# Optimization experiments

Hardware: AMD Instinct MI355X
Metric: run time of the kernel (lower is better)

Reference implementation:

```python
import jax, jax.numpy as jnp
import numpy as np

NUM_GAUSS = 64
MAX_R = 5.0
ANG_TO_NM = 0.1  # du.ANG_TO_NM_SCALE
L = 4
C_NODE = 256
C_HID = 256
MAX_ATOMS = 100
B = 512      # building blocks
NPB = 32     # atoms per block
K = 20       # max_neighbors
N = B * NPB
E = N * K
GAUSS_COEFF = -0.5 / (MAX_R / (NUM_GAUSS - 1)) ** 2


def setup_inputs() -> dict:
    rng = np.random.default_rng(0)
    # all atoms of a block inside a 2.5A cube -> every pair within MAX_R=5A,
    # so radius_graph capped at K neighbors == K-nearest graph (fixed E).
    pos = (rng.random((B, NPB, 3)) * 2.5).astype(np.float32)
    d = np.linalg.norm(pos[:, :, None, :] - pos[:, None, :, :], axis=-1)  # [B,n,n]
    ii = np.arange(NPB)
    d[:, ii, ii] = np.inf  # loop=False
    nbr = np.argsort(d, axis=-1)[:, :, :K]  # [B,n,K] nearest neighbors
    base = (np.arange(B) * NPB)[:, None, None]
    row = np.broadcast_to(ii[None, :, None], (B, NPB, K)) + base
    col = nbr + base
    edge_index = np.stack([row.reshape(-1), col.reshape(-1)]).astype(np.int64)

    key = jax.random.key(0)
    ks = jax.random.split(key, 8)

    def lin(k, fi, fo):
        return jax.random.normal(k, (L, fi, fo), jnp.float32) / np.sqrt(fi).astype(np.float32)

    d_e_in = 2 * C_NODE + 1 + NUM_GAUSS  # 577
    return {
        'local_coords': jnp.asarray(pos.reshape(N, 3)),
        'atom_types': jax.random.randint(ks[0], (N,), 1, MAX_ATOMS + 1),  # 1..max_atoms
        'edge_index': jnp.asarray(edge_index),
        'batch_bb': jnp.repeat(jnp.arange(B, dtype=jnp.int32), NPB),
        'atom_embed': jax.random.normal(ks[1], (MAX_ATOMS, C_NODE), jnp.float32) * 0.1,
        'offset': jnp.linspace(0.0, MAX_R, NUM_GAUSS, dtype=jnp.float32),
        'We1': lin(ks[2], d_e_in, C_HID), 'be1': jnp.zeros((L, C_HID), jnp.float32),
        'We2': lin(ks[3], C_HID, C_HID), 'be2': jnp.zeros((L, C_HID), jnp.float32),
        'Wn1': lin(ks[4], C_HID + C_NODE, C_HID), 'bn1': jnp.zeros((L, C_HID), jnp.float32),
        'Wn2': lin(ks[5], C_HID, C_NODE), 'bn2': jnp.zeros((L, C_NODE), jnp.float32),
    }


def _forward(local_coords, atom_types, edge_index, batch_bb, atom_embed, offset,
             We1, be1, We2, be2, Wn1, bn1, Wn2, bn2):
    row, col = edge_index[0], edge_index[1]
    h = atom_embed[atom_types - 1]                      # [N, C_NODE]
    # Gaussian smearing of pairwise distances (Angstrom)
    dvec = local_coords[col] - local_coords[row]        # [E, 3]
    dist = jnp.sqrt(jnp.sum(dvec * dvec, axis=-1))      # [E]
    edge_attr = jnp.exp(GAUSS_COEFF * (dist[:, None] - offset[None, :]) ** 2)  # [E, 64]
    coord = local_coords * ANG_TO_NM
    cdiff = coord[row] - coord[col]
    radial = jnp.sum(cdiff * cdiff, axis=-1, keepdims=True)  # [E, 1]
    nblocks = batch_bb.shape[0] // NPB  # static
    for l in range(L):  # small fixed layer count
        e_in = jnp.concatenate([h[row], h[col], radial, edge_attr], axis=-1)  # [E, 577]
        m = jax.nn.relu(e_in @ We1[l] + be1[l])
        m = jax.nn.relu(m @ We2[l] + be2[l])                 # edge_mlp output [E, C_HID]
        agg = jax.ops.segment_sum(m, row, num_segments=N)    # scatter-sum to nodes
        n_in = jnp.concatenate([h, agg], axis=-1)            # [N, C_NODE + C_HID]
        out = jax.nn.relu(n_in @ Wn1[l] + bn1[l]) @ Wn2[l] + bn2[l]
        node_update = h + out                                # residual inside E_GCL
        h = h + node_update                                  # outer residual in forward
    # global_mean_pool over building blocks
    s = jax.ops.segment_sum(h, batch_bb, num_segments=B)
    cnt = jax.ops.segment_sum(jnp.ones((h.shape[0], 1), h.dtype), batch_bb, num_segments=B)
    return s / cnt


def reference(local_coords, atom_types, edge_index, batch_bb, atom_embed, offset,
              We1, be1, We2, be2, Wn1, bn1, Wn2, bn2):
    return _forward(local_coords, atom_types, edge_index, batch_bb, atom_embed, offset,
                    We1, be1, We2, be2, Wn1, bn1, Wn2, bn2)
```

## Files before the change

kernel.cpp:

```cpp
#include <hip/hip_runtime.h>
#include <hip/hip_bf16.h>
#include <stdint.h>

#define NATOMS 16384
#define ETOT   327680
#define NLAYER 4

typedef __hip_bfloat16 bf16;
using bf16x8 = __attribute__((ext_vector_type(8))) short;
using f32x4  = __attribute__((ext_vector_type(4))) float;

#define LDSF_STRIDE 260
#define WBR_STRIDE  66

__device__ __forceinline__ float bf2f(short s) {
  union { float f; unsigned u; } x; x.u = ((unsigned)(unsigned short)s) << 16; return x.f;
}
__device__ __forceinline__ short f2bf(float f) {
  bf16 b = __float2bfloat16(f);
  return *(short*)&b;
}

__device__ __forceinline__ void async16(const void* g, void* l) {
  __builtin_amdgcn_global_load_lds(
      (const __attribute__((address_space(1))) unsigned int*)g,
      (__attribute__((address_space(3))) unsigned int*)l, 16, 0, 0);
}

template<int KTOT, int EPI, int MT>
__global__ void __launch_bounds__(256, 2)
gemm_k(const bf16* A, const bf16* A2, const bf16* B,
       bf16* Obf, int ldOut, const float* bias,
       float* Hf, bf16* Hbf)
{
  __shared__ __align__(16) char smem[49152];
  __shared__ float s_bias[256];

  const int tid  = threadIdx.x;
  const int w    = tid >> 6;
  const int lane = tid & 63;
  const int q    = lane >> 4;
  const int t16  = lane & 15;
  const size_t row0 = (size_t)blockIdx.x * MT;
  const int ncol0 = blockIdx.y * 256;
  constexpr int MI = MT / 16;
  constexpr int AI = MT / 32;

  if constexpr (EPI == 2 || EPI == 4) s_bias[tid] = bias[tid];

  f32x4 acc[MI][4] = {};

  constexpr int NCHUNK = KTOT / 64;
  for (int kc = 0; kc < NCHUNK; ++kc) {
    const int k0 = kc * 64;
    const bf16* Asrc; int k0e; int ldA;
    if constexpr (KTOT == 512) {
      if (k0 < 256) { Asrc = A;  k0e = k0;       }
      else          { Asrc = A2; k0e = k0 - 256; }
      ldA = 256;
    } else {
      Asrc = A; k0e = k0; ldA = KTOT;
    }

    __syncthreads();
    #pragma unroll
    for (int ii = 0; ii < AI; ++ii) {
      int i = w * AI + ii;
      int f = i * 64 + lane;
      int m = f >> 3, s = f & 7;
      int ko = s ^ (m & 7);
      const bf16* g = Asrc + (row0 + (size_t)m) * ldA + (size_t)(k0e + ko * 8);
      async16(g, smem + i * 1024);
    }
    #pragma unroll
    for (int ii = 0; ii < 8; ++ii) {
      int i = w * 8 + ii;
      int f = i * 64 + lane;
      int n = f >> 3, s = f & 7;
      int ko = s ^ (n & 7);
      const bf16* g = B + (size_t)(ncol0 + n) * KTOT + (size_t)(k0 + ko * 8);
      async16(g, smem + 16384 + i * 1024);
    }
    __syncthreads();

    #pragma unroll
    for (int ks = 0; ks < 2; ++ks) {
      bf16x8 av[MI]; bf16x8 bv[4];
      const int ko = q + 4 * ks;
      #pragma unroll
      for (int mi = 0; mi < MI; ++mi) {
        int m = 16 * mi + t16;
        int f = m * 8 + (ko ^ (m & 7));
        av[mi] = *(const bf16x8*)(smem + f * 16);
      }
      #pragma unroll
      for (int ni = 0; ni < 4; ++ni) {
        int n = 64 * w + 16 * ni + t16;
        int f = n * 8 + (ko ^ (n & 7));
        bv[ni] = *(const bf16x8*)(smem + 16384 + f * 16);
      }
      #pragma unroll
      for (int mi = 0; mi < MI; ++mi)
        #pragma unroll
        for (int ni = 0; ni < 4; ++ni)
          acc[mi][ni] = __builtin_amdgcn_mfma_f32_16x16x32_bf16(
              av[mi], bv[ni], acc[mi][ni], 0, 0, 0);
    }
  }

  float* lds_f = (float*)smem;
  #pragma unroll
  for (int mi = 0; mi < MI; ++mi) {
    __syncthreads();
    #pragma unroll
    for (int ni = 0; ni < 4; ++ni)
      #pragma unroll
      for (int r = 0; r < 4; ++r)
        lds_f[(4 * q + r) * LDSF_STRIDE + 64 * w + 16 * ni + t16] = acc[mi][ni][r];
    __syncthreads();
    #pragma unroll
    for (int j = 0; j < 2; ++j) {
      int task = tid + 256 * j;
      int rr = task >> 5, cg = task & 31;
      int c0 = cg * 8;
      size_t rg = row0 + 16 * mi + rr;
      f32x4 v0 = *(const f32x4*)(lds_f + rr * LDSF_STRIDE + c0);
      f32x4 v1 = *(const f32x4*)(lds_f + rr * LDSF_STRIDE + c0 + 4);
      float v[8] = {v0[0], v0[1], v0[2], v0[3], v1[0], v1[1], v1[2], v1[3]};
      if constexpr (EPI == 0) {
        bf16x8 o;
        #pragma unroll
        for (int k = 0; k < 8; ++k) o[k] = f2bf(v[k]);
        *(bf16x8*)(Obf + rg * ldOut + (ncol0 + c0)) = o;
      } else if constexpr (EPI == 2) {
        bf16x8 o;
        #pragma unroll
        for (int k = 0; k < 8; ++k) o[k] = f2bf(fmaxf(v[k] + s_bias[c0 + k], 0.f));
        *(bf16x8*)(Obf + rg * 256 + c0) = o;
      } else {
        f32x4 h0 = *(const f32x4*)(Hf + rg * 256 + c0);
        f32x4 h1 = *(const f32x4*)(Hf + rg * 256 + c0 + 4);
        float hh[8] = {h0[0], h0[1], h0[2], h0[3], h1[0], h1[1], h1[2], h1[3]};
        bf16x8 o; f32x4 n0, n1;
        #pragma unroll
        for (int k = 0; k < 8; ++k) {
          float hn = 2.f * hh[k] + v[k] + s_bias[c0 + k];
          o[k] = f2bf(hn);
          if (k < 4) n0[k] = hn; else n1[k - 4] = hn;
        }
        *(f32x4*)(Hf + rg * 256 + c0)     = n0;
        *(f32x4*)(Hf + rg * 256 + c0 + 4) = n1;
        *(bf16x8*)(Hbf + rg * 256 + c0) = o;
      }
    }
  }
}

#define M1OFF 0
#define BREG  40960
__global__ void __launch_bounds__(256, 2)
edge_fused(const bf16* WgT_l, const bf16* We2T_l, const float* off,
           const float* pos, const int* eidx, const bf16* Prc,
           const float* be1, const float* wrad, const float* be2, bf16* Agg)
{
  __shared__ __align__(16) char smem[73728];
  __shared__ int   s_erow[80];
  __shared__ int   s_ecol[80];
  __shared__ float s_rad[80];
  __shared__ float s_dist[80];
  __shared__ float s_b1[256];
  __shared__ float s_wrad[256];
  __shared__ float s_b2[256];
  __shared__ float s_off[64];

  const int tid  = threadIdx.x;
  const int w    = tid >> 6;
  const int lane = tid & 63;
  const int q    = lane >> 4;
  const int t16  = lane & 15;
  const size_t erow0 = (size_t)blockIdx.x * 80;

  if (tid < 80) {
    int e = (int)erow0 + tid;
    int r = eidx[e], c = eidx[ETOT + e];
    float dx = pos[c * 3 + 0] - pos[r * 3 + 0];
    float dy = pos[c * 3 + 1] - pos[r * 3 + 1];
    float dz = pos[c * 3 + 2] - pos[r * 3 + 2];
    float d2 = dx * dx + dy * dy + dz * dz;
    s_erow[tid] = r; s_ecol[tid] = c;
    s_rad[tid]  = 0.01f * d2;
    s_dist[tid] = sqrtf(d2);
  }
  if (tid < 64) s_off[tid] = off[tid];
  s_b1[tid]   = be1[tid];
  s_wrad[tid] = wrad[tid];
  s_b2[tid]   = be2[tid];

  #pragma unroll
  for (int ii = 0; ii < 8; ++ii) {
    int i = w * 8 + ii;
    int f = i * 64 + lane;
    int n = f >> 3, s = f & 7;
    int ko = s ^ (n & 7);
    async16(WgT_l + (size_t)n * 64 + ko * 8, smem + BREG + i * 1024);
  }
  __syncthreads();

  const float GC = -0.5f / ((5.0f / 63.0f) * (5.0f / 63.0f));
  float offk[2][8];
  #pragma unroll
  for (int ks = 0; ks < 2; ++ks)
    #pragma unroll
    for (int j = 0; j < 8; ++j) offk[ks][j] = s_off[(q + 4 * ks) * 8 + j];

  bf16x8 ag[5][2];
  #pragma unroll
  for (int mi = 0; mi < 5; ++mi) {
    float d = s_dist[16 * mi + t16];
    #pragma unroll
    for (int ks = 0; ks < 2; ++ks)
      #pragma unroll
      for (int j = 0; j < 8; ++j) {
        float t = d - offk[ks][j];
        ag[mi][ks][j] = f2bf(__expf(GC * t * t));
      }
  }

  f32x4 acc1[5][4] = {};
  #pragma unroll
  for (int ks = 0; ks < 2; ++ks) {
    bf16x8 bv[4];
    const int ko = q + 4 * ks;
    #pragma unroll
    for (int ni = 0; ni < 4; ++ni) {
      int n = 64 * w + 16 * ni + t16;
      int f = n * 8 + (ko ^ (n & 7));
      bv[ni] = *(const bf16x8*)(smem + BREG + f * 16);
    }
    #pragma unroll
    for (int mi = 0; mi < 5; ++mi)
      #pragma unroll
      for (int ni = 0; ni < 4; ++ni)
        acc1[mi][ni] = __builtin_amdgcn_mfma_f32_16x16x32_bf16(
            ag[mi][ks], bv[ni], acc1[mi][ni], 0, 0, 0);
  }

  {
    float* br = (float*)(smem + BREG + 8192 * w);
    const int rs = lane >> 3, oct = lane & 7;
    const int c0e = 64 * w + oct * 8;
    float b18[8], wr8[8];
    #pragma unroll
    for (int k = 0; k < 8; ++k) { b18[k] = s_b1[c0e + k]; wr8[k] = s_wrad[c0e + k]; }

    #pragma unroll
    for (int mi = 0; mi < 5; ++mi) {
      #pragma unroll
      for (int ni = 0; ni < 4; ++ni)
        #pragma unroll
        for (int r = 0; r < 4; ++r)
          br[(4 * q + r) * WBR_STRIDE + 16 * ni + t16] = acc1[mi][ni][r];
      #pragma unroll
      for (int pass = 0; pass < 2; ++pass) {
        int rr = pass * 8 + rs;
        int rl = 16 * mi + rr;
        int er = s_erow[rl], ec = s_ecol[rl];
        float rad = s_rad[rl];
        bf16x8 pr = *(const bf16x8*)(Prc + (size_t)er * 512 + c0e);
        bf16x8 pc = *(const bf16x8*)(Prc + (size_t)ec * 512 + 256 + c0e);
        float v[8];
        #pragma unroll
        for (int jj = 0; jj < 4; ++jj) {
          float2 t = *(const float2*)(br + rr * WBR_STRIDE + oct * 8 + 2 * jj);
          v[2 * jj] = t.x; v[2 * jj + 1] = t.y;
        }
        bf16x8 o;
        #pragma unroll
        for (int k = 0; k < 8; ++k) {
          float val = v[k] + b18[k] + rad * wr8[k] + bf2f(pr[k]) + bf2f(pc[k]);
          o[k] = f2bf(fmaxf(val, 0.f));
        }
        int od = (8 * w + oct) ^ (rl & 7);
        *(bf16x8*)(smem + rl * 512 + od * 16) = o;
      }
    }
  }
  __syncthreads();

  f32x4 acc2[5][4] = {};
  for (int kc = 0; kc < 4; ++kc) {
    if (kc) __syncthreads();
    #pragma unroll
    for (int ii = 0; ii < 8; ++ii) {
      int i = w * 8 + ii;
      int f = i * 64 + lane;
      int n = f >> 3, s = f & 7;
      int ko = s ^ (n & 7);
      async16(We2T_l + (size_t)n * 256 + (size_t)(64 * kc + ko * 8),
              smem + BREG + i * 1024);
    }
    __syncthreads();

    #pragma unroll
    for (int ks = 0; ks < 2; ++ks) {
      bf16x8 av[5]; bf16x8 bv[4];
      const int ko = q + 4 * ks;
      #pragma unroll
      for (int mi = 0; mi < 5; ++mi) {
        int m = 16 * mi + t16;
        int oa = (8 * kc + ko) ^ (t16 & 7);
        av[mi] = *(const bf16x8*)(smem + m * 512 + oa * 16);
      }
      #pragma unroll
      for (int ni = 0; ni < 4; ++ni) {
        int n = 64 * w + 16 * ni + t16;
        int f = n * 8 + (ko ^ (n & 7));
        bv[ni] = *(const bf16x8*)(smem + BREG + f * 16);
      }
      #pragma unroll
      for (int mi = 0; mi < 5; ++mi)
        #pragma unroll
        for (int ni = 0; ni < 4; ++ni)
          acc2[mi][ni] = __builtin_amdgcn_mfma_f32_16x16x32_bf16(
              av[mi], bv[ni], acc2[mi][ni], 0, 0, 0);
    }
  }

  #pragma unroll
  for (int ni = 0; ni < 4; ++ni) {
    float b = s_b2[64 * w + 16 * ni + t16];
    float pp[5];
    #pragma unroll
    for (int mi = 0; mi < 5; ++mi) {
      float s = 0.f;
      #pragma unroll
      for (int r = 0; r < 4; ++r) s += fmaxf(acc2[mi][ni][r] + b, 0.f);
      pp[mi] = s;
    }
    #pragma unroll
    for (int nn = 0; nn < 4; ++nn) {
      float s = 0.f;
      #pragma unroll
      for (int mi = 0; mi < 5; ++mi) {
        int g = 4 * mi + q;
        if (g >= 5 * nn && g <= 5 * nn + 4) s += pp[mi];
      }
      s += __shfl_xor(s, 16, 64);
      s += __shfl_xor(s, 32, 64);
      if (q == nn)
        Agg[((size_t)blockIdx.x * 4 + nn) * 256 + 64 * w + 16 * ni + t16] =
            __float2bfloat16(s);
    }
  }
}

__global__ void wrct_kernel(const float* We1, bf16* WrcT) {
  int idx = blockIdx.x * 256 + threadIdx.x;
  int k = idx & 255, np = (idx >> 8) & 511, l = idx >> 17;
  float v = (np < 256)
      ? We1[((size_t)l * 577 + k) * 256 + np]
      : We1[((size_t)l * 577 + 256 + k) * 256 + (np - 256)];
  WrcT[idx] = __float2bfloat16(v);
}
__global__ void wgt_kernel(const float* We1, bf16* WgT) {
  int idx = blockIdx.x * 256 + threadIdx.x;
  int k = idx & 63, n = (idx >> 6) & 255, l = idx >> 14;
  WgT[idx] = __float2bfloat16(We1[((size_t)l * 577 + 513 + k) * 256 + n]);
}
__global__ void wrad_kernel(const float* We1, float* wrad) {
  int idx = blockIdx.x * 256 + threadIdx.x;
  int n = idx & 255, l = idx >> 8;
  wrad[idx] = We1[((size_t)l * 577 + 512) * 256 + n];
}
__global__ void trans_kernel(const float* src, bf16* dst, int R, int C) {
  int idx = blockIdx.x * 256 + threadIdx.x;
  int k = idx % R, rest = idx / R;
  int n = rest % C, l = rest / C;
  dst[idx] = __float2bfloat16(src[((size_t)l * R + k) * C + n]);
}

__global__ void h0_kernel(const int* types, const float* emb, float* h, bf16* hbf) {
  int i = blockIdx.x, c = threadIdx.x;
  float v = emb[(size_t)(types[i] - 1) * 256 + c];
  h[(size_t)i * 256 + c] = v;
  hbf[(size_t)i * 256 + c] = __float2bfloat16(v);
}

__global__ void pool_kernel(const float* h, float* out) {
  int b = blockIdx.x, c = threadIdx.x;
  float s = 0.f;
  #pragma unroll
  for (int j = 0; j < 32; ++j) s += h[((size_t)b * 32 + j) * 256 + c];
  out[(size_t)b * 256 + c] = s * (1.0f / 32.0f);
}

extern "C" void kernel_launch(void* const* d_in, const int* in_sizes, int n_in,
                              void* d_out, int out_size, void* d_ws, size_t ws_size,
                              hipStream_t stream) {
  const float* pos   = (const float*)d_in[0];
  const int*   atype = (const int*)  d_in[1];
  const int*   eidx  = (const int*)  d_in[2];
  const float* emb   = (const float*)d_in[4];
  const float* off   = (const float*)d_in[5];
  const float* We1   = (const float*)d_in[6];
  const float* be1   = (const float*)d_in[7];
  const float* We2   = (const float*)d_in[8];
  const float* be2   = (const float*)d_in[9];
  const float* Wn1   = (const float*)d_in[10];
  const float* bn1   = (const float*)d_in[11];
  const float* Wn2   = (const float*)d_in[12];
  const float* bn2   = (const float*)d_in[13];
  float* out = (float*)d_out;

  size_t o = 0;
  auto carve = [&](size_t bytes) {
    void* p = (char*)d_ws + o;
    o += (bytes + 255) & ~(size_t)255;
    return p;
  };
  float* h     = (float*)carve((size_t)NATOMS * 256 * 4);
  bf16*  hbf   = (bf16*) carve((size_t)NATOMS * 256 * 2);
  bf16*  Prc   = (bf16*) carve((size_t)NATOMS * 512 * 2);
  bf16*  aggbf = (bf16*) carve((size_t)NATOMS * 256 * 2);
  bf16*  WrcT  = (bf16*) carve((size_t)NLAYER * 512 * 256 * 2);
  bf16*  WgT   = (bf16*) carve((size_t)NLAYER * 256 * 64 * 2);
  bf16*  We2T  = (bf16*) carve((size_t)NLAYER * 256 * 256 * 2);
  bf16*  Wn1T  = (bf16*) carve((size_t)NLAYER * 256 * 512 * 2);
  bf16*  Wn2T  = (bf16*) carve((size_t)NLAYER * 256 * 256 * 2);
  float* wradp = (float*)carve((size_t)NLAYER * 256 * 4);

  wrct_kernel<<<2048, 256, 0, stream>>>(We1, WrcT);
  wgt_kernel <<< 256, 256, 0, stream>>>(We1, WgT);
  wrad_kernel<<<   4, 256, 0, stream>>>(We1, wradp);
  trans_kernel<<<1024, 256, 0, stream>>>(We2, We2T, 256, 256);
  trans_kernel<<<2048, 256, 0, stream>>>(Wn1, Wn1T, 512, 256);
  trans_kernel<<<1024, 256, 0, stream>>>(Wn2, Wn2T, 256, 256);
  h0_kernel  <<<NATOMS, 256, 0, stream>>>(atype, emb, h, hbf);

  for (int l = 0; l < NLAYER; ++l) {
    gemm_k<256, 0, 64><<<dim3(256, 2), 256, 0, stream>>>(
        hbf, nullptr, WrcT + (size_t)l * 512 * 256, Prc, 512, nullptr,
        nullptr, nullptr);
    edge_fused<<<ETOT / 80, 256, 0, stream>>>(
        WgT + (size_t)l * 256 * 64, We2T + (size_t)l * 256 * 256, off, pos,
        eidx, Prc, be1 + l * 256, wradp + l * 256, be2 + l * 256, aggbf);
    gemm_k<512, 2, 64><<<dim3(256, 1), 256, 0, stream>>>(
        hbf, aggbf, Wn1T + (size_t)l * 256 * 512, aggbf, 256, bn1 + l * 256,
        nullptr, nullptr);
    gemm_k<256, 4, 64><<<dim3(256, 1), 256, 0, stream>>>(
        aggbf, nullptr, Wn2T + (size_t)l * 256 * 256, nullptr, 0, bn2 + l * 256,
        h, hbf);
  }

  pool_kernel<<<512, 256, 0, stream>>>(h, out);
}
```

Baseline: 645.4 us.

## Load edge-MLP weights straight into registers and shrink LDS for higher occupancy

The edge_fused kernel stops staging the Gaussian weight matrix and the We2 tiles through LDS. Each wave now reads its weight fragments directly from global memory into registers. The first GEMM is transposed so that its accumulator layout matches the epilogue, which removes the fp32 round-trip through LDS; Gaussian features are written to LDS once instead. LDS drops from 72KB to 40KB and launch bounds rise to 3 blocks per CU, aiming for more occupancy and fewer barriers, at the cost of more per-wave global weight loads and higher register pressure.

```diff
diff --git a/kernel.cpp b/kernel.cpp
--- a/kernel.cpp
+++ b/kernel.cpp
@@ -8,10 +8,10 @@
 
 typedef __hip_bfloat16 bf16;
 using bf16x8 = __attribute__((ext_vector_type(8))) short;
+using bf16x4 = __attribute__((ext_vector_type(4))) short;
 using f32x4  = __attribute__((ext_vector_type(4))) float;
 
 #define LDSF_STRIDE 260
-#define WBR_STRIDE  66
 
 __device__ __forceinline__ float bf2f(short s) {
   union { float f; unsigned u; } x; x.u = ((unsigned)(unsigned short)s) << 16; return x.f;
@@ -156,14 +156,12 @@
   }
 }
 
-#define M1OFF 0
-#define BREG  40960
-__global__ void __launch_bounds__(256, 2)
+__global__ void __launch_bounds__(256, 3)
 edge_fused(const bf16* WgT_l, const bf16* We2T_l, const float* off,
            const float* pos, const int* eidx, const bf16* Prc,
            const float* be1, const float* wrad, const float* be2, bf16* Agg)
 {
-  __shared__ __align__(16) char smem[73728];
+  __shared__ __align__(16) char smem[40960];
   __shared__ int   s_erow[80];
   __shared__ int   s_ecol[80];
   __shared__ float s_rad[80];
@@ -179,6 +177,16 @@
   const int q    = lane >> 4;
   const int t16  = lane & 15;
   const size_t erow0 = (size_t)blockIdx.x * 80;
+
+  bf16x8 wgf[4][2];
+  #pragma unroll
+  for (int fi = 0; fi < 4; ++fi)
+    #pragma unroll
+    for (int ks = 0; ks < 2; ++ks) {
+      int feat = 64 * w + 16 * fi + t16;
+      int ko = q + 4 * ks;
+      wgf[fi][ks] = *(const bf16x8*)(WgT_l + (size_t)feat * 64 + ko * 8);
+    }
 
   if (tid < 80) {
     int e = (int)erow0 + tid;
@@ -195,93 +203,73 @@
   s_b1[tid]   = be1[tid];
   s_wrad[tid] = wrad[tid];
   s_b2[tid]   = be2[tid];
-
-  #pragma unroll
-  for (int ii = 0; ii < 8; ++ii) {
-    int i = w * 8 + ii;
-    int f = i * 64 + lane;
-    int n = f >> 3, s = f & 7;
-    int ko = s ^ (n & 7);
-    async16(WgT_l + (size_t)n * 64 + ko * 8, smem + BREG + i * 1024);
-  }
   __syncthreads();
 
-  const float GC = -0.5f / ((5.0f / 63.0f) * (5.0f / 63.0f));
-  float offk[2][8];
-  #pragma unroll
-  for (int ks = 0; ks < 2; ++ks)
-    #pragma unroll
-    for (int j = 0; j < 8; ++j) offk[ks][j] = s_off[(q + 4 * ks) * 8 + j];
-
-  bf16x8 ag[5][2];
-  #pragma unroll
-  for (int mi = 0; mi < 5; ++mi) {
-    float d = s_dist[16 * mi + t16];
-    #pragma unroll
-    for (int ks = 0; ks < 2; ++ks)
+  {
+    const float GC = -0.5f / ((5.0f / 63.0f) * (5.0f / 63.0f));
+    for (int idx = tid; idx < 640; idx += 256) {
+      int e = idx >> 3, oct = idx & 7;
+      float d = s_dist[e];
+      bf16x8 v;
       #pragma unroll
       for (int j = 0; j < 8; ++j) {
-        float t = d - offk[ks][j];
-        ag[mi][ks][j] = f2bf(__expf(GC * t * t));
-      }
-  }
-
-  f32x4 acc1[5][4] = {};
+        float t = d - s_off[oct * 8 + j];
+        v[j] = f2bf(__expf(GC * t * t));
+      }
+      int f = e * 8 + (oct ^ (e & 7));
+      *(bf16x8*)(smem + f * 16) = v;
+    }
+  }
+  __syncthreads();
+
+  f32x4 acc1[4][5] = {};
   #pragma unroll
   for (int ks = 0; ks < 2; ++ks) {
-    bf16x8 bv[4];
     const int ko = q + 4 * ks;
-    #pragma unroll
-    for (int ni = 0; ni < 4; ++ni) {
-      int n = 64 * w + 16 * ni + t16;
-      int f = n * 8 + (ko ^ (n & 7));
-      bv[ni] = *(const bf16x8*)(smem + BREG + f * 16);
-    }
-    #pragma unroll
-    for (int mi = 0; mi < 5; ++mi)
-      #pragma unroll
-      for (int ni = 0; ni < 4; ++ni)
-        acc1[mi][ni] = __builtin_amdgcn_mfma_f32_16x16x32_bf16(
-            ag[mi][ks], bv[ni], acc1[mi][ni], 0, 0, 0);
-  }
+    bf16x8 gv[5];
+    #pragma unroll
+    for (int ci = 0; ci < 5; ++ci) {
+      int e = 16 * ci + t16;
+      int f = e * 8 + (ko ^ (e & 7));
+      gv[ci] = *(const bf16x8*)(smem + f * 16);
+    }
+    #pragma unroll
+    for (int fi = 0; fi < 4; ++fi)
+      #pragma unroll
+      for (int ci = 0; ci < 5; ++ci)
+        acc1[fi][ci] = __builtin_amdgcn_mfma_f32_16x16x32_bf16(
+            wgf[fi][ks], gv[ci], acc1[fi][ci], 0, 0, 0);
+  }
+  __syncthreads();
 
   {
-    float* br = (float*)(smem + BREG + 8192 * w);
-    const int rs = lane >> 3, oct = lane & 7;
-    const int c0e = 64 * w + oct * 8;
-    float b18[8], wr8[8];
-    #pragma unroll
-    for (int k = 0; k < 8; ++k) { b18[k] = s_b1[c0e + k]; wr8[k] = s_wrad[c0e + k]; }
-
-    #pragma unroll
-    for (int mi = 0; mi < 5; ++mi) {
-      #pragma unroll
-      for (int ni = 0; ni < 4; ++ni)
-        #pragma unroll
-        for (int r = 0; r < 4; ++r)
-          br[(4 * q + r) * WBR_STRIDE + 16 * ni + t16] = acc1[mi][ni][r];
-      #pragma unroll
-      for (int pass = 0; pass < 2; ++pass) {
-        int rr = pass * 8 + rs;
-        int rl = 16 * mi + rr;
-        int er = s_erow[rl], ec = s_ecol[rl];
-        float rad = s_rad[rl];
-        bf16x8 pr = *(const bf16x8*)(Prc + (size_t)er * 512 + c0e);
-        bf16x8 pc = *(const bf16x8*)(Prc + (size_t)ec * 512 + 256 + c0e);
-        float v[8];
-        #pragma unroll
-        for (int jj = 0; jj < 4; ++jj) {
-          float2 t = *(const float2*)(br + rr * WBR_STRIDE + oct * 8 + 2 * jj);
-          v[2 * jj] = t.x; v[2 * jj + 1] = t.y;
+    float b1r[4][4], wrr[4][4];
+    #pragma unroll
+    for (int fi = 0; fi < 4; ++fi) {
+      f32x4 tb = *(const f32x4*)(s_b1 + 64 * w + 16 * fi + 4 * q);
+      f32x4 tw = *(const f32x4*)(s_wrad + 64 * w + 16 * fi + 4 * q);
+      #pragma unroll
+      for (int r = 0; r < 4; ++r) { b1r[fi][r] = tb[r]; wrr[fi][r] = tw[r]; }
+    }
+    #pragma unroll
+    for (int ci = 0; ci < 5; ++ci) {
+      int e = 16 * ci + t16;
+      int er = s_erow[e], ec = s_ecol[e];
+      float rad = s_rad[e];
+      #pragma unroll
+      for (int fi = 0; fi < 4; ++fi) {
+        int fb = 64 * w + 16 * fi + 4 * q;
+        bf16x4 pr = *(const bf16x4*)(Prc + (size_t)er * 512 + fb);
+        bf16x4 pc = *(const bf16x4*)(Prc + (size_t)ec * 512 + 256 + fb);
+        bf16x4 o;
+        #pragma unroll
+        for (int r = 0; r < 4; ++r) {
+          float val = acc1[fi][ci][r] + b1r[fi][r] + rad * wrr[fi][r]
+                    + bf2f(pr[r]) + bf2f(pc[r]);
+          o[r] = f2bf(fmaxf(val, 0.f));
         }
-        bf16x8 o;
-        #pragma unroll
-        for (int k = 0; k < 8; ++k) {
-          float val = v[k] + b18[k] + rad * wr8[k] + bf2f(pr[k]) + bf2f(pc[k]);
-          o[k] = f2bf(fmaxf(val, 0.f));
-        }
-        int od = (8 * w + oct) ^ (rl & 7);
-        *(bf16x8*)(smem + rl * 512 + od * 16) = o;
+        int u = (16 * w + 4 * fi + q) ^ (e & 14);
+        *(bf16x4*)(smem + e * 512 + u * 8) = o;
       }
     }
   }
@@ -289,40 +277,31 @@
 
   f32x4 acc2[5][4] = {};
   for (int kc = 0; kc < 4; ++kc) {
-    if (kc) __syncthreads();
-    #pragma unroll
-    for (int ii = 0; ii < 8; ++ii) {
-      int i = w * 8 + ii;
-      int f = i * 64 + lane;
-      int n = f >> 3, s = f & 7;
-      int ko = s ^ (n & 7);
-      async16(We2T_l + (size_t)n * 256 + (size_t)(64 * kc + ko * 8),
-              smem + BREG + i * 1024);
-    }
-    __syncthreads();
-
+    bf16x8 bv[4][2];
+    #pragma unroll
+    for (int ni = 0; ni < 4; ++ni)
+      #pragma unroll
+      for (int ks = 0; ks < 2; ++ks) {
+        int n = 64 * w + 16 * ni + t16;
+        int ko = q + 4 * ks;
+        bv[ni][ks] = *(const bf16x8*)(We2T_l + (size_t)n * 256 + kc * 64 + ko * 8);
+      }
     #pragma unroll
     for (int ks = 0; ks < 2; ++ks) {
-      bf16x8 av[5]; bf16x8 bv[4];
       const int ko = q + 4 * ks;
+      bf16x8 av[5];
       #pragma unroll
       for (int mi = 0; mi < 5; ++mi) {
-        int m = 16 * mi + t16;
-        int oa = (8 * kc + ko) ^ (t16 & 7);
-        av[mi] = *(const bf16x8*)(smem + m * 512 + oa * 16);
-      }
-      #pragma unroll
-      for (int ni = 0; ni < 4; ++ni) {
-        int n = 64 * w + 16 * ni + t16;
-        int f = n * 8 + (ko ^ (n & 7));
-        bv[ni] = *(const bf16x8*)(smem + BREG + f * 16);
+        int e = 16 * mi + t16;
+        int ub = (2 * (8 * kc + ko)) ^ (t16 & 14);
+        av[mi] = *(const bf16x8*)(smem + e * 512 + ub * 8);
       }
       #pragma unroll
       for (int mi = 0; mi < 5; ++mi)
         #pragma unroll
         for (int ni = 0; ni < 4; ++ni)
           acc2[mi][ni] = __builtin_amdgcn_mfma_f32_16x16x32_bf16(
-              av[mi], bv[ni], acc2[mi][ni], 0, 0, 0);
+              av[mi], bv[ni][ks], acc2[mi][ni], 0, 0, 0);
     }
   }
 
```

Measured after the change: 751.7 us. +16.5%, slower.
